# Kernel tuning notes

Hardware: AMD Instinct MI355X
Metric: run time of the kernel (lower is better)

The kernel has to match this reference:

```python
import jax, jax.numpy as jnp
import numpy as np

N_NODES = 100000
N_EDGES = 3200000
N_GRAPHS = 1024
D = 64
STEPS_PROP = 6
STEPS_S2S = 6


def setup_inputs() -> dict:
    key = jax.random.key(0)
    ks = jax.random.split(key, 16)
    inp = {}
    inp['x'] = jax.random.normal(ks[0], (N_NODES, 15), dtype=jnp.float32)
    inp['edge_index'] = jax.random.randint(ks[1], (2, N_EDGES), 0, N_NODES, dtype=jnp.int64 if jax.config.jax_enable_x64 else jnp.int32)
    inp['batch'] = jnp.sort(jax.random.randint(ks[2], (N_NODES,), 0, N_GRAPHS, dtype=jnp.int64 if jax.config.jax_enable_x64 else jnp.int32))
    s = 0.1
    inp['W0'] = jax.random.normal(ks[3], (15, D), dtype=jnp.float32) * s
    inp['b0'] = jax.random.normal(ks[4], (D,), dtype=jnp.float32) * s
    inp['Wc'] = jax.random.normal(ks[5], (D, D), dtype=jnp.float32) * s
    inp['bc'] = jax.random.normal(ks[6], (D,), dtype=jnp.float32) * s
    inp['Wih'] = jax.random.normal(ks[7], (4 * D, 2 * D), dtype=jnp.float32) * s
    inp['Whh'] = jax.random.normal(ks[8], (4 * D, D), dtype=jnp.float32) * s
    inp['bih'] = jax.random.normal(ks[9], (4 * D,), dtype=jnp.float32) * s
    inp['bhh'] = jax.random.normal(ks[10], (4 * D,), dtype=jnp.float32) * s
    inp['W1'] = jax.random.normal(ks[11], (2 * D, D), dtype=jnp.float32) * s
    inp['b1'] = jax.random.normal(ks[12], (D,), dtype=jnp.float32) * s
    inp['W2'] = jax.random.normal(ks[13], (D, 12), dtype=jnp.float32) * s
    inp['b2'] = jax.random.normal(ks[14], (12,), dtype=jnp.float32) * s
    return inp


def _gcn_forward(x, edge_index, batch, W0, b0, Wc, bc, Wih, Whh, bih, bhh, W1, b1, W2, b2):
    N = x.shape[0]
    # GCNConv normalization with self-loops (PyG semantics): A_hat = D^-1/2 (A+I) D^-1/2
    loops = jnp.arange(N, dtype=edge_index.dtype)
    row = jnp.concatenate([edge_index[0], loops])  # source
    col = jnp.concatenate([edge_index[1], loops])  # target
    deg = jax.ops.segment_sum(jnp.ones_like(col, dtype=x.dtype), col, num_segments=N)
    dinv = jnp.where(deg > 0, jax.lax.rsqrt(jnp.maximum(deg, 1e-30)), 0.0)
    norm = dinv[row] * dinv[col]  # [E+N]

    out = jax.nn.relu(x @ W0 + b0)  # [N, D]
    for _ in range(STEPS_PROP):
        h = out @ Wc  # transform first
        msg = h[row] * norm[:, None]  # gather along edges
        out = jax.nn.relu(jax.ops.segment_sum(msg, col, num_segments=N) + bc)

    # Set2Set pooling
    B = N_GRAPHS
    d = out.shape[1]
    h_l = jnp.zeros((B, d), dtype=out.dtype)
    c_l = jnp.zeros((B, d), dtype=out.dtype)
    q_star = jnp.zeros((B, 2 * d), dtype=out.dtype)
    for _ in range(STEPS_S2S):
        gates = q_star @ Wih.T + h_l @ Whh.T + bih + bhh  # [B, 4d]
        i_g, f_g, g_g, o_g = jnp.split(gates, 4, axis=1)
        c_l = jax.nn.sigmoid(f_g) * c_l + jax.nn.sigmoid(i_g) * jnp.tanh(g_g)
        h_l = jax.nn.sigmoid(o_g) * jnp.tanh(c_l)
        q = h_l  # [B, d]
        e = jnp.sum(out * q[batch], axis=-1)  # [N]
        m = jax.ops.segment_max(e, batch, num_segments=B)
        a_num = jnp.exp(e - m[batch])
        denom = jax.ops.segment_sum(a_num, batch, num_segments=B)
        a = a_num / denom[batch]
        r = jax.ops.segment_sum(a[:, None] * out, batch, num_segments=B)  # [B, d]
        q_star = jnp.concatenate([q, r], axis=-1)

    y = jax.nn.relu(q_star @ W1 + b1)
    return y @ W2 + b2  # [B, 12]


def reference(x, edge_index, batch, W0, b0, Wc, bc, Wih, Whh, bih, bhh, W1, b1, W2, b2):
    return _gcn_forward(x, edge_index, batch, W0, b0, Wc, bc, Wih, Whh, bih, bhh, W1, b1, W2, b2)
```

## Files before the change

### kernel.cpp

```cpp
#include <hip/hip_runtime.h>
#include <hip/hip_fp16.h>
#include <math.h>

#define ND 64
constexpr int BKT_SHIFT = 9;
constexpr int BKT_MASK = (1 << BKT_SHIFT) - 1;
constexpr int BCUR_PAD = 16;
constexpr int STG_TILE = 8192;

__device__ __forceinline__ float sigmoidf_(float x){ return 1.f/(1.f+__expf(-x)); }
__device__ __forceinline__ __half2 h2lo(uint2 v){ return *reinterpret_cast<__half2*>(&v.x); }
__device__ __forceinline__ __half2 h2hi(uint2 v){ return *reinterpret_cast<__half2*>(&v.y); }
__device__ __forceinline__ __half2 shxor_h2(__half2 h, int off){
  unsigned u = *reinterpret_cast<unsigned*>(&h);
  u = __shfl_xor(u, off, 64);
  return *reinterpret_cast<__half2*>(&u);
}

__global__ void k_bhist(const int* __restrict__ col, int* __restrict__ bgcnt,
                        int E, int NBK){
  __shared__ int lhist[512];
  int t0 = blockIdx.x * STG_TILE;
  int t1 = t0 + STG_TILE; if (t1 > E) t1 = E;
  for (int i = threadIdx.x; i < NBK; i += 256) lhist[i] = 0;
  __syncthreads();
  for (int i = t0 + threadIdx.x; i < t1; i += 256)
    atomicAdd(&lhist[col[i] >> BKT_SHIFT], 1);
  __syncthreads();
  for (int i = threadIdx.x; i < NBK; i += 256)
    if (lhist[i] > 0) atomicAdd(&bgcnt[i], lhist[i]);
}

__global__ void k_bscan(const int* __restrict__ bgcnt, int* __restrict__ bstart,
                        int* __restrict__ rowptr, int NBK, int E, int N){
  __shared__ int tmp[256];
  int t = threadIdx.x;
  int v = (t < NBK) ? bgcnt[t] : 0;
  tmp[t] = v; __syncthreads();
  for (int off=1; off<256; off<<=1){
    int u = (t>=off) ? tmp[t-off] : 0;
    __syncthreads();
    tmp[t] += u;
    __syncthreads();
  }
  if (t <= NBK) bstart[t] = (t==0) ? 0 : tmp[t-1];
  if (t == 0) rowptr[N] = E;
}

__global__ void k_bcinit(const int* __restrict__ bstart, int* __restrict__ bcur, int NBK){
  int b = blockIdx.x*blockDim.x + threadIdx.x;
  if (b < NBK) bcur[b*BCUR_PAD] = bstart[b];
}

__global__ void k_stage2(const int* __restrict__ row, const int* __restrict__ col,
                         int* __restrict__ bcur, unsigned* __restrict__ pairs,
                         int E, int NBK){
  __shared__ int lhist[512];
  __shared__ int lbase[512];
  int t0 = blockIdx.x * STG_TILE;
  int t1 = t0 + STG_TILE; if (t1 > E) t1 = E;
  for (int i = threadIdx.x; i < NBK; i += 256) lhist[i] = 0;
  __syncthreads();
  for (int i = t0 + threadIdx.x; i < t1; i += 256)
    atomicAdd(&lhist[col[i] >> BKT_SHIFT], 1);
  __syncthreads();
  for (int i = threadIdx.x; i < NBK; i += 256){
    int c = lhist[i];
    lbase[i] = (c > 0) ? atomicAdd(&bcur[i*BCUR_PAD], c) : 0;
    lhist[i] = 0;
  }
  __syncthreads();
  for (int i = t0 + threadIdx.x; i < t1; i += 256){
    int d = col[i];
    int b = d >> BKT_SHIFT;
    int pos = lbase[b] + atomicAdd(&lhist[b], 1);
    pairs[pos] = ((unsigned)row[i] << BKT_SHIFT) | (unsigned)(d & BKT_MASK);
  }
}

__global__ void k_place(const unsigned* __restrict__ pairs, const int* __restrict__ bstart,
                        int* __restrict__ rowptr, float* __restrict__ dinv,
                        int* __restrict__ csr, int N){
  __shared__ int h[1 << BKT_SHIFT];
  __shared__ int excl[1 << BKT_SHIFT];
  __shared__ int tsum[256];
  int b = blockIdx.x;
  int base = b << BKT_SHIFT;
  int nend = base + (1 << BKT_SHIFT); if (nend > N) nend = N;
  int cnt = nend - base;
  int t = threadIdx.x;
  int s = bstart[b], e = bstart[b+1];

  h[2*t] = 0; h[2*t+1] = 0;
  __syncthreads();
  for (int i = s + t; i < e; i += 256)
    atomicAdd(&h[pairs[i] & BKT_MASK], 1);
  __syncthreads();
  int a0 = h[2*t], a1 = h[2*t+1];
  tsum[t] = a0 + a1;
  __syncthreads();
  for (int off=1; off<256; off<<=1){
    int u = (t>=off) ? tsum[t-off] : 0;
    __syncthreads();
    tsum[t] += u;
    __syncthreads();
  }
  int base0 = (t==0) ? 0 : tsum[t-1];
  excl[2*t]   = base0;
  excl[2*t+1] = base0 + a0;
  __syncthreads();
  for (int c = t; c < cnt; c += 256){
    int deg = h[c];
    rowptr[base + c] = s + excl[c];
    dinv[base + c] = rsqrtf((float)(deg + 1));
  }
  __syncthreads();
  for (int c = t; c < cnt; c += 256) h[c] = s + excl[c];
  __syncthreads();
  for (int i = s + t; i < e; i += 256){
    unsigned p = pairs[i];
    int pos = atomicAdd(&h[p & BKT_MASK], 1);
    csr[pos] = (int)(p >> BKT_SHIFT);
  }
}

__global__ void k_input(const float* __restrict__ x, const float* __restrict__ W0,
                        const float* __restrict__ b0, const float* __restrict__ dinv,
                        __half* __restrict__ s, int N){
  __shared__ float w0s[15*ND];
  __shared__ float b0s[ND];
  int tid = threadIdx.x;
  for (int i=tid; i<15*ND; i+=256) w0s[i] = W0[i];
  if (tid < ND) b0s[tid] = b0[tid];
  __syncthreads();
  int node = blockIdx.x*4 + (tid>>6);
  int f = tid & 63;
  if (node < N){
    float acc = b0s[f];
    const float* xr = x + (size_t)node*15;
    #pragma unroll
    for (int k=0;k<15;k++) acc += xr[k]*w0s[k*ND+f];
    s[(size_t)node*ND+f] = __float2half_rn(dinv[node]*fmaxf(acc, 0.f));
  }
}

__global__ void k_prop(const __half* __restrict__ sbuf, const int* __restrict__ rowptr,
                       const int* __restrict__ csr, const float* __restrict__ dinv,
                       const float* __restrict__ Wc, const float* __restrict__ bc,
                       __half* __restrict__ s_new, __half* __restrict__ outh,
                       int N, int wout){
  __shared__ float wcs[ND*ND];
  __shared__ float xs[16][ND];
  __shared__ float bcs[ND];
  const uint2* g8 = (const uint2*)sbuf;
  int tid = threadIdx.x;
  for (int i=tid; i<ND*ND; i+=256) wcs[i] = Wc[i];
  if (tid < ND) bcs[tid] = bc[tid];
  int nb = blockIdx.x*16;
  int wv = tid>>6, lane = tid&63;
  int grp = lane>>4, li = lane&15;

  for (int q=0; q<4; ++q){
    int node = nb + wv*4 + q;
    float val = 0.f;
    if (node < N){
      int s = rowptr[node], e = rowptr[node+1];
      __half2 z = __float2half2_rn(0.f);
      __half2 a0x=z,a0y=z, a1x=z,a1y=z, a2x=z,a2y=z, a3x=z,a3y=z;
      int i = s;
      for (; i + 16 <= e; i += 16){
        int s0 = csr[i +  0 + grp];
        int s1 = csr[i +  4 + grp];
        int s2 = csr[i +  8 + grp];
        int s3 = csr[i + 12 + grp];
        uint2 v0 = g8[(size_t)s0*16 + li];
        uint2 v1 = g8[(size_t)s1*16 + li];
        uint2 v2 = g8[(size_t)s2*16 + li];
        uint2 v3 = g8[(size_t)s3*16 + li];
        a0x = __hadd2(a0x, h2lo(v0)); a0y = __hadd2(a0y, h2hi(v0));
        a1x = __hadd2(a1x, h2lo(v1)); a1y = __hadd2(a1y, h2hi(v1));
        a2x = __hadd2(a2x, h2lo(v2)); a2y = __hadd2(a2y, h2hi(v2));
        a3x = __hadd2(a3x, h2lo(v3)); a3y = __hadd2(a3y, h2hi(v3));
      }
      for (; i + 4 <= e; i += 4){
        int s0 = csr[i + grp];
        uint2 v0 = g8[(size_t)s0*16 + li];
        a0x = __hadd2(a0x, h2lo(v0)); a0y = __hadd2(a0y, h2hi(v0));
      }
      int r = e - i;
      if (grp < r){
        int s0 = csr[i + grp];
        uint2 v0 = g8[(size_t)s0*16 + li];
        a1x = __hadd2(a1x, h2lo(v0)); a1y = __hadd2(a1y, h2hi(v0));
      }
      __half2 sxh = __hadd2(__hadd2(a0x,a1x), __hadd2(a2x,a3x));
      __half2 syh = __hadd2(__hadd2(a0y,a1y), __hadd2(a2y,a3y));
      sxh = __hadd2(sxh, shxor_h2(sxh, 16));
      syh = __hadd2(syh, shxor_h2(syh, 16));
      sxh = __hadd2(sxh, shxor_h2(sxh, 32));
      syh = __hadd2(syh, shxor_h2(syh, 32));
      uint2 sv = g8[(size_t)node*16 + li];
      sxh = __hadd2(sxh, h2lo(sv));
      syh = __hadd2(syh, h2hi(sv));
      val = (grp==0) ? __half2float(__low2half(sxh))
          : (grp==1) ? __half2float(__high2half(sxh))
          : (grp==2) ? __half2float(__low2half(syh))
          :            __half2float(__high2half(syh));
    }
    xs[wv*4+q][4*li+grp] = val;
  }
  __syncthreads();

  int f = tid&63, nq = tid>>6;
  float acc0=0.f, acc1=0.f, acc2=0.f, acc3=0.f;
  #pragma unroll 16
  for (int k=0;k<ND;k++){
    float w = wcs[k*ND+f];
    acc0 += w*xs[nq*4+0][k];
    acc1 += w*xs[nq*4+1][k];
    acc2 += w*xs[nq*4+2][k];
    acc3 += w*xs[nq*4+3][k];
  }
  int n0 = nb + nq*4;
  float bcf = bcs[f];
  #pragma unroll
  for (int j=0; j<4; ++j){
    int node = n0 + j;
    if (node < N){
      float a = (j==0)?acc0:(j==1)?acc1:(j==2)?acc2:acc3;
      float dn = dinv[node];
      float r = fmaxf(dn*a + bcf, 0.f);
      s_new[(size_t)node*ND+f] = __float2half_rn(dn*r);
      if (wout) outh[(size_t)node*ND+f] = __float2half_rn(r);
    }
  }
}

__global__ void k_goff(const int* __restrict__ batch, int* __restrict__ goff, int N, int B){
  int i = blockIdx.x*blockDim.x + threadIdx.x;
  if (i >= N) return;
  int b = batch[i];
  if (i == 0){ for (int g2=0; g2<=b; ++g2) goff[g2]=0; }
  else {
    int bp = batch[i-1];
    for (int g2=bp+1; g2<=b; ++g2) goff[g2]=i;
  }
  if (i == N-1){ for (int g2=b+1; g2<=B; ++g2) goff[g2]=N; }
}

__global__ void k_lstm(const float* __restrict__ Wih, const float* __restrict__ Whh,
                       const float* __restrict__ bih, const float* __restrict__ bhh,
                       float* __restrict__ qs, float* __restrict__ hl, float* __restrict__ cl){
  __shared__ float qsr[8][128];
  __shared__ float hlr[8][64];
  __shared__ float gat[8][256];
  int tid = threadIdx.x;
  int g0 = blockIdx.x*8;
  for (int i=tid; i<8*128; i+=256){ int gg=i>>7, k=i&127; qsr[gg][k] = qs[(size_t)(g0+gg)*128+k]; }
  for (int i=tid; i<8*64;  i+=256){ int gg=i>>6, k=i&63;  hlr[gg][k] = hl[(size_t)(g0+gg)*64+k]; }
  __syncthreads();
  int j = tid;
  float bb = bih[j] + bhh[j];
  float acc[8];
  #pragma unroll
  for (int gg=0; gg<8; gg++) acc[gg] = bb;
  const float* wr = Wih + (size_t)j*128;
  for (int k=0; k<128; k++){
    float w = wr[k];
    #pragma unroll
    for (int gg=0; gg<8; gg++) acc[gg] += w*qsr[gg][k];
  }
  const float* wr2 = Whh + (size_t)j*64;
  for (int k=0; k<64; k++){
    float w = wr2[k];
    #pragma unroll
    for (int gg=0; gg<8; gg++) acc[gg] += w*hlr[gg][k];
  }
  #pragma unroll
  for (int gg=0; gg<8; gg++) gat[gg][j] = acc[gg];
  __syncthreads();
  #pragma unroll
  for (int it=0; it<2; ++it){
    int idx = it*256 + tid;
    int gg = idx>>6, d = idx&63;
    int graph = g0+gg;
    float ig = sigmoidf_(gat[gg][d]);
    float fg = sigmoidf_(gat[gg][64+d]);
    float gv = tanhf(gat[gg][128+d]);
    float og = sigmoidf_(gat[gg][192+d]);
    float c = fg*cl[(size_t)graph*64+d] + ig*gv;
    float h = og*tanhf(c);
    cl[(size_t)graph*64+d] = c;
    hl[(size_t)graph*64+d] = h;
    qs[(size_t)graph*128+d] = h;
  }
}

__global__ void k_attn(const __half* __restrict__ out, const int* __restrict__ goff,
                       const float* __restrict__ hl, float* __restrict__ qs){
  __shared__ float redm[4], redd[4];
  __shared__ float redr[4][64];
  int g = blockIdx.x;
  int tid = threadIdx.x, lane = tid&63, wv = tid>>6;
  int s = goff[g], e = goff[g+1];
  float q = hl[(size_t)g*64+lane];
  float m = -3.0e38f, denom = 0.f, racc = 0.f;
  for (int n=s+wv; n<e; n+=4){
    float v = __half2float(out[(size_t)n*64+lane]);
    float p = v*q;
    #pragma unroll
    for (int off=32; off>=1; off>>=1) p += __shfl_xor(p, off, 64);
    if (p > m){
      float sc = __expf(m - p);
      denom *= sc; racc *= sc; m = p;
    }
    float w = __expf(p - m);
    denom += w; racc += w*v;
  }
  if (lane==0){ redm[wv] = m; redd[wv] = denom; }
  redr[wv][lane] = racc;
  __syncthreads();
  if (wv==0){
    float m0=redm[0], m1=redm[1], m2=redm[2], m3=redm[3];
    float mm = fmaxf(fmaxf(m0,m1), fmaxf(m2,m3));
    float s0=__expf(m0-mm), s1=__expf(m1-mm), s2=__expf(m2-mm), s3=__expf(m3-mm);
    float dt = redd[0]*s0 + redd[1]*s1 + redd[2]*s2 + redd[3]*s3;
    float rs = redr[0][lane]*s0 + redr[1][lane]*s1 + redr[2][lane]*s2 + redr[3][lane]*s3;
    qs[(size_t)g*128+64+lane] = (dt > 0.f) ? rs/dt : 0.f;
  }
}

__global__ void k_final(const float* __restrict__ qs, const float* __restrict__ W1,
                        const float* __restrict__ b1, const float* __restrict__ W2,
                        const float* __restrict__ b2, float* __restrict__ outy){
  __shared__ float qsr[128];
  __shared__ float yy[64];
  int g = blockIdx.x; int t = threadIdx.x;
  qsr[t]    = qs[(size_t)g*128 + t];
  qsr[64+t] = qs[(size_t)g*128 + 64 + t];
  __syncthreads();
  float acc = b1[t];
  for (int k=0; k<128; k++) acc += qsr[k]*W1[k*64+t];
  yy[t] = fmaxf(acc, 0.f);
  __syncthreads();
  if (t < 12){
    float a2 = b2[t];
    for (int k=0; k<64; k++) a2 += yy[k]*W2[k*12+t];
    outy[(size_t)g*12 + t] = a2;
  }
}

extern "C" void kernel_launch(void* const* d_in, const int* in_sizes, int n_in,
                              void* d_out, int out_size, void* d_ws, size_t ws_size,
                              hipStream_t stream){
  const float* x    = (const float*)d_in[0];
  const int*   ei   = (const int*)d_in[1];
  const int*   batch= (const int*)d_in[2];
  const float* W0   = (const float*)d_in[3];
  const float* b0   = (const float*)d_in[4];
  const float* Wc   = (const float*)d_in[5];
  const float* bc   = (const float*)d_in[6];
  const float* Wih  = (const float*)d_in[7];
  const float* Whh  = (const float*)d_in[8];
  const float* bih  = (const float*)d_in[9];
  const float* bhh  = (const float*)d_in[10];
  const float* W1   = (const float*)d_in[11];
  const float* b1   = (const float*)d_in[12];
  const float* W2   = (const float*)d_in[13];
  const float* b2   = (const float*)d_in[14];
  float* yout = (float*)d_out;

  const int N = in_sizes[0]/15;
  const int E = in_sizes[1]/2;
  const int B = out_size/12;
  const int NBK = (N + (1<<BKT_SHIFT) - 1) >> BKT_SHIFT;
  const int* row = ei;
  const int* col = ei + E;

  char* ws = (char*)d_ws;
  size_t off = 0;
  auto alloc = [&](size_t bytes)->void*{
    void* p = ws + off; off = (off + bytes + 255) & ~(size_t)255; return p;
  };
  int*      bgcnt   = (int*)     alloc((size_t)(NBK+1)*4);
  int*      bstart  = (int*)     alloc((size_t)(NBK+1)*4);
  int*      bcur    = (int*)     alloc((size_t)NBK*BCUR_PAD*4);
  int*      rowptr  = (int*)     alloc((size_t)(N+1)*4);
  unsigned* pairs   = (unsigned*)alloc((size_t)E*4);
  int*      csr     = (int*)     alloc((size_t)E*4);
  float*    dinv    = (float*)   alloc((size_t)N*4);
  __half*   nodef   = (__half*)  alloc((size_t)N*ND*2);
  __half*   s_a     = (__half*)  alloc((size_t)N*ND*2);
  __half*   s_b     = (__half*)  alloc((size_t)N*ND*2);
  int*      goff    = (int*)     alloc((size_t)(B+1)*4);
  float*    hl      = (float*)   alloc((size_t)B*64*4);
  float*    cl      = (float*)   alloc((size_t)B*64*4);
  float*    qs      = (float*)   alloc((size_t)B*128*4);
  (void)ws_size; (void)n_in;

  hipMemsetAsync(bgcnt, 0, (size_t)(NBK+1)*4, stream);
  hipMemsetAsync(hl,   0, (size_t)B*64*4, stream);
  hipMemsetAsync(cl,   0, (size_t)B*64*4, stream);
  hipMemsetAsync(qs,   0, (size_t)B*128*4, stream);

  int nstg = (E + STG_TILE - 1)/STG_TILE;
  k_bhist <<<nstg, 256, 0, stream>>>(col, bgcnt, E, NBK);
  k_bscan <<<1, 256, 0, stream>>>(bgcnt, bstart, rowptr, NBK, E, N);
  k_bcinit<<<(NBK+255)/256, 256, 0, stream>>>(bstart, bcur, NBK);
  k_stage2<<<nstg, 256, 0, stream>>>(row, col, bcur, pairs, E, NBK);
  k_place <<<NBK, 256, 0, stream>>>(pairs, bstart, rowptr, dinv, csr, N);

  k_input<<<(N+3)/4, 256, 0, stream>>>(x, W0, b0, dinv, s_a, N);
  __half* scur = s_a; __half* snxt = s_b;
  for (int s6=0; s6<6; ++s6){
    k_prop<<<(N+15)/16, 256, 0, stream>>>(scur, rowptr, csr, dinv,
                                          Wc, bc, snxt, nodef, N, (s6==5)?1:0);
    __half* t = scur; scur = snxt; snxt = t;
  }

  k_goff<<<(N+255)/256, 256, 0, stream>>>(batch, goff, N, B);
  for (int s6=0; s6<6; ++s6){
    k_lstm<<<B/8, 256, 0, stream>>>(Wih, Whh, bih, bhh, qs, hl, cl);
    k_attn<<<B,   256, 0, stream>>>(nodef, goff, hl, qs);
  }
  k_final<<<B, 64, 0, stream>>>(qs, W1, b1, W2, b2, yout);
}
```

Before: 921.2 us.

## Fuse Set2Set LSTM, attention and readout into one persistent kernel per graph pair

Replaces the 13 separate launches (six LSTM, six attention, one final MLP) with a single kernel in which each block owns two graphs. The block keeps the LSTM state and q_star in shared memory across all six steps and then runs the final MLP in place. This removes launch overhead, the global round trips of hl/cl/qs and three memsets. The last propagation step now skips writing s_new when it writes the node features. In exchange, the LSTM weights are re-read per block for every step with only two graphs of reuse, attention uses two waves per graph instead of four, and only 512 blocks are launched.

```diff
diff --git a/kernel.cpp b/kernel.cpp
--- a/kernel.cpp
+++ b/kernel.cpp
@@ -230,8 +230,8 @@
       float a = (j==0)?acc0:(j==1)?acc1:(j==2)?acc2:acc3;
       float dn = dinv[node];
       float r = fmaxf(dn*a + bcf, 0.f);
-      s_new[(size_t)node*ND+f] = __float2half_rn(dn*r);
       if (wout) outh[(size_t)node*ND+f] = __float2half_rn(r);
+      else      s_new[(size_t)node*ND+f] = __float2half_rn(dn*r);
     }
   }
 }
@@ -248,105 +248,87 @@
   if (i == N-1){ for (int g2=b+1; g2<=B; ++g2) goff[g2]=N; }
 }
 
-__global__ void k_lstm(const float* __restrict__ Wih, const float* __restrict__ Whh,
-                       const float* __restrict__ bih, const float* __restrict__ bhh,
-                       float* __restrict__ qs, float* __restrict__ hl, float* __restrict__ cl){
-  __shared__ float qsr[8][128];
-  __shared__ float hlr[8][64];
-  __shared__ float gat[8][256];
+__global__ void k_s2s(const __half* __restrict__ nodef, const int* __restrict__ goff,
+                      const float* __restrict__ Wih, const float* __restrict__ Whh,
+                      const float* __restrict__ bih, const float* __restrict__ bhh,
+                      const float* __restrict__ W1, const float* __restrict__ b1,
+                      const float* __restrict__ W2, const float* __restrict__ b2,
+                      float* __restrict__ outy, int B){
+  __shared__ float qsr[2][128];
+  __shared__ float hlr[2][64];
+  __shared__ float clr[2][64];
+  __shared__ float gat[2][256];
+  __shared__ float redm[2][2], redd[2][2];
+  __shared__ float redr[2][2][64];
+  __shared__ float yy[2][64];
   int tid = threadIdx.x;
-  int g0 = blockIdx.x*8;
-  for (int i=tid; i<8*128; i+=256){ int gg=i>>7, k=i&127; qsr[gg][k] = qs[(size_t)(g0+gg)*128+k]; }
-  for (int i=tid; i<8*64;  i+=256){ int gg=i>>6, k=i&63;  hlr[gg][k] = hl[(size_t)(g0+gg)*64+k]; }
-  __syncthreads();
-  int j = tid;
-  float bb = bih[j] + bhh[j];
-  float acc[8];
-  #pragma unroll
-  for (int gg=0; gg<8; gg++) acc[gg] = bb;
-  const float* wr = Wih + (size_t)j*128;
-  for (int k=0; k<128; k++){
-    float w = wr[k];
-    #pragma unroll
-    for (int gg=0; gg<8; gg++) acc[gg] += w*qsr[gg][k];
-  }
-  const float* wr2 = Whh + (size_t)j*64;
-  for (int k=0; k<64; k++){
-    float w = wr2[k];
-    #pragma unroll
-    for (int gg=0; gg<8; gg++) acc[gg] += w*hlr[gg][k];
-  }
-  #pragma unroll
-  for (int gg=0; gg<8; gg++) gat[gg][j] = acc[gg];
-  __syncthreads();
-  #pragma unroll
-  for (int it=0; it<2; ++it){
-    int idx = it*256 + tid;
-    int gg = idx>>6, d = idx&63;
-    int graph = g0+gg;
-    float ig = sigmoidf_(gat[gg][d]);
-    float fg = sigmoidf_(gat[gg][64+d]);
-    float gv = tanhf(gat[gg][128+d]);
-    float og = sigmoidf_(gat[gg][192+d]);
-    float c = fg*cl[(size_t)graph*64+d] + ig*gv;
-    float h = og*tanhf(c);
-    cl[(size_t)graph*64+d] = c;
-    hl[(size_t)graph*64+d] = h;
-    qs[(size_t)graph*128+d] = h;
-  }
-}
-
-__global__ void k_attn(const __half* __restrict__ out, const int* __restrict__ goff,
-                       const float* __restrict__ hl, float* __restrict__ qs){
-  __shared__ float redm[4], redd[4];
-  __shared__ float redr[4][64];
-  int g = blockIdx.x;
-  int tid = threadIdx.x, lane = tid&63, wv = tid>>6;
-  int s = goff[g], e = goff[g+1];
-  float q = hl[(size_t)g*64+lane];
-  float m = -3.0e38f, denom = 0.f, racc = 0.f;
-  for (int n=s+wv; n<e; n+=4){
-    float v = __half2float(out[(size_t)n*64+lane]);
-    float p = v*q;
-    #pragma unroll
-    for (int off=32; off>=1; off>>=1) p += __shfl_xor(p, off, 64);
-    if (p > m){
-      float sc = __expf(m - p);
-      denom *= sc; racc *= sc; m = p;
+  int g0 = blockIdx.x*2;
+  if (g0 >= B) return;
+  for (int i=tid;i<2*128;i+=256) qsr[i>>7][i&127]=0.f;
+  if (tid<128){ hlr[tid>>6][tid&63]=0.f; clr[tid>>6][tid&63]=0.f; }
+  __syncthreads();
+  int lane=tid&63, wv=tid>>6;
+  int gg_w = wv>>1, wp = wv&1;
+  for (int step=0; step<6; ++step){
+    float bb = bih[tid]+bhh[tid];
+    float a0=bb, a1=bb;
+    const float* wr = Wih + (size_t)tid*128;
+    for (int k=0;k<128;k++){ float w=wr[k]; a0+=w*qsr[0][k]; a1+=w*qsr[1][k]; }
+    const float* wr2 = Whh + (size_t)tid*64;
+    for (int k=0;k<64;k++){ float w=wr2[k]; a0+=w*hlr[0][k]; a1+=w*hlr[1][k]; }
+    gat[0][tid]=a0; gat[1][tid]=a1;
+    __syncthreads();
+    if (tid<128){
+      int gg=tid>>6, d=tid&63;
+      float ig=sigmoidf_(gat[gg][d]);
+      float fg=sigmoidf_(gat[gg][64+d]);
+      float gv=tanhf(gat[gg][128+d]);
+      float og=sigmoidf_(gat[gg][192+d]);
+      float c = fg*clr[gg][d]+ig*gv;
+      float h = og*tanhf(c);
+      clr[gg][d]=c; hlr[gg][d]=h; qsr[gg][d]=h;
     }
-    float w = __expf(p - m);
-    denom += w; racc += w*v;
-  }
-  if (lane==0){ redm[wv] = m; redd[wv] = denom; }
-  redr[wv][lane] = racc;
-  __syncthreads();
-  if (wv==0){
-    float m0=redm[0], m1=redm[1], m2=redm[2], m3=redm[3];
-    float mm = fmaxf(fmaxf(m0,m1), fmaxf(m2,m3));
-    float s0=__expf(m0-mm), s1=__expf(m1-mm), s2=__expf(m2-mm), s3=__expf(m3-mm);
-    float dt = redd[0]*s0 + redd[1]*s1 + redd[2]*s2 + redd[3]*s3;
-    float rs = redr[0][lane]*s0 + redr[1][lane]*s1 + redr[2][lane]*s2 + redr[3][lane]*s3;
-    qs[(size_t)g*128+64+lane] = (dt > 0.f) ? rs/dt : 0.f;
-  }
-}
-
-__global__ void k_final(const float* __restrict__ qs, const float* __restrict__ W1,
-                        const float* __restrict__ b1, const float* __restrict__ W2,
-                        const float* __restrict__ b2, float* __restrict__ outy){
-  __shared__ float qsr[128];
-  __shared__ float yy[64];
-  int g = blockIdx.x; int t = threadIdx.x;
-  qsr[t]    = qs[(size_t)g*128 + t];
-  qsr[64+t] = qs[(size_t)g*128 + 64 + t];
-  __syncthreads();
-  float acc = b1[t];
-  for (int k=0; k<128; k++) acc += qsr[k]*W1[k*64+t];
-  yy[t] = fmaxf(acc, 0.f);
-  __syncthreads();
-  if (t < 12){
-    float a2 = b2[t];
-    for (int k=0; k<64; k++) a2 += yy[k]*W2[k*12+t];
-    outy[(size_t)g*12 + t] = a2;
+    __syncthreads();
+    {
+      int g = g0+gg_w;
+      int s = goff[g], e = goff[g+1];
+      float q = hlr[gg_w][lane];
+      float m=-3.0e38f, denom=0.f, racc=0.f;
+      for (int n=s+wp; n<e; n+=2){
+        float v = __half2float(nodef[(size_t)n*64+lane]);
+        float p = v*q;
+        #pragma unroll
+        for (int off=32; off>=1; off>>=1) p += __shfl_xor(p, off, 64);
+        if (p>m){ float sc=__expf(m-p); denom*=sc; racc*=sc; m=p; }
+        float w=__expf(p-m);
+        denom+=w; racc+=w*v;
+      }
+      if (lane==0){ redm[gg_w][wp]=m; redd[gg_w][wp]=denom; }
+      redr[gg_w][wp][lane]=racc;
+    }
+    __syncthreads();
+    if (wp==0){
+      float m0=redm[gg_w][0], m1=redm[gg_w][1];
+      float mm=fmaxf(m0,m1);
+      float s0=__expf(m0-mm), s1=__expf(m1-mm);
+      float dt=redd[gg_w][0]*s0+redd[gg_w][1]*s1;
+      float rs=redr[gg_w][0][lane]*s0+redr[gg_w][1][lane]*s1;
+      qsr[gg_w][64+lane] = (dt>0.f)? rs/dt : 0.f;
+    }
+    __syncthreads();
+  }
+  if (tid<128){
+    int gg=tid>>6, f=tid&63;
+    float acc=b1[f];
+    for (int k=0;k<128;k++) acc += qsr[gg][k]*W1[k*64+f];
+    yy[gg][f]=fmaxf(acc,0.f);
+  }
+  __syncthreads();
+  if (tid<24){
+    int gg=tid/12, o=tid%12;
+    float a2=b2[o];
+    for (int k=0;k<64;k++) a2 += yy[gg][k]*W2[k*12+o];
+    outy[(size_t)(g0+gg)*12+o]=a2;
   }
 }
 
@@ -393,15 +375,9 @@
   __half*   s_a     = (__half*)  alloc((size_t)N*ND*2);
   __half*   s_b     = (__half*)  alloc((size_t)N*ND*2);
   int*      goff    = (int*)     alloc((size_t)(B+1)*4);
-  float*    hl      = (float*)   alloc((size_t)B*64*4);
-  float*    cl      = (float*)   alloc((size_t)B*64*4);
-  float*    qs      = (float*)   alloc((size_t)B*128*4);
   (void)ws_size; (void)n_in;
 
   hipMemsetAsync(bgcnt, 0, (size_t)(NBK+1)*4, stream);
-  hipMemsetAsync(hl,   0, (size_t)B*64*4, stream);
-  hipMemsetAsync(cl,   0, (size_t)B*64*4, stream);
-  hipMemsetAsync(qs,   0, (size_t)B*128*4, stream);
 
   int nstg = (E + STG_TILE - 1)/STG_TILE;
   k_bhist <<<nstg, 256, 0, stream>>>(col, bgcnt, E, NBK);
@@ -419,9 +395,6 @@
   }
 
   k_goff<<<(N+255)/256, 256, 0, stream>>>(batch, goff, N, B);
-  for (int s6=0; s6<6; ++s6){
-    k_lstm<<<B/8, 256, 0, stream>>>(Wih, Whh, bih, bhh, qs, hl, cl);
-    k_attn<<<B,   256, 0, stream>>>(nodef, goff, hl, qs);
-  }
-  k_final<<<B, 64, 0, stream>>>(qs, W1, b1, W2, b2, yout);
-}
+  k_s2s<<<(B+1)/2, 256, 0, stream>>>(nodef, goff, Wih, Whh, bih, bhh,
+                                     W1, b1, W2, b2, yout, B);
+}
```

Result: no change. 937.7 us (+1.8%).
